# Performance work log

Hardware: AMD Instinct MI355X
Metric: run time of the kernel (lower is better)

## Reference

```python
import jax, jax.numpy as jnp
import numpy as np

HEADS = 8
DIM_HEAD = 64


def setup_inputs() -> dict:
    key = jax.random.key(0)
    ks = jax.random.split(key, 8)
    B, L, m = 4, 1024, 64
    Dq, Dc = 512, 256
    inner = HEADS * DIM_HEAD  # 512
    x = jax.random.normal(ks[0], (B, L, Dq), dtype=jnp.float32)
    context = jax.random.normal(ks[1], (B, L, m, Dc), dtype=jnp.float32)
    mask = jax.random.randint(ks[2], (B, L, m), 0, 2).astype(bool)
    # guarantee at least one valid token per (b,l) row
    mask = mask.at[:, :, 0].set(True)
    bias = jax.random.normal(ks[3], (B, L, m), dtype=jnp.float32)
    s = 0.02
    Wq = jax.random.normal(ks[4], (Dq, inner), dtype=jnp.float32) * s
    Wk = jax.random.normal(ks[5], (Dc, inner), dtype=jnp.float32) * s
    Wv = jax.random.normal(ks[6], (Dc, inner), dtype=jnp.float32) * s
    Wo = jax.random.normal(ks[7], (inner, Dq), dtype=jnp.float32) * s
    bo = jnp.zeros((Dq,), dtype=jnp.float32)
    return {"x": x, "context": context, "mask": mask, "bias": bias,
            "Wq": Wq, "Wk": Wk, "Wv": Wv, "Wo": Wo, "bo": bo}


def reference(x, context, mask, bias, Wq, Wk, Wv, Wo, bo):
    B, L, Dq = x.shape
    m = context.shape[2]
    scale = DIM_HEAD ** (-0.5)
    # projections
    Q = (x @ Wq).reshape(B, L, HEADS, DIM_HEAD)                 # b l h d
    K = (context @ Wk).reshape(B, L, m, HEADS, DIM_HEAD)        # b l m h d
    V = (context @ Wv).reshape(B, L, m, HEADS, DIM_HEAD)        # b l m h d
    scores = jnp.einsum('blhd,blmhd->blhm', Q, K) * scale       # b l h m
    scores = scores + bias[:, :, None, :]
    scores = jnp.where(mask[:, :, None, :], scores, -jnp.inf)
    attn = jax.nn.softmax(scores, axis=-1)
    out = jnp.einsum('blhm,blmhd->blhd', attn, V).reshape(B, L, HEADS * DIM_HEAD)
    return out @ Wo + bo
```

## Files before the change

### kernel.cpp

```cpp
#include <hip/hip_runtime.h>
#include <cstddef>


typedef __attribute__((ext_vector_type(8))) short short8;
typedef __attribute__((ext_vector_type(4))) float float4v;

__device__ __forceinline__ short f2bf(float f) {
  unsigned u = __float_as_uint(f);
  return (short)((u + 0x7fffu + ((u >> 16) & 1u)) >> 16);
}

__global__ __launch_bounds__(256) void k_prep(const float* __restrict__ x,
                                              const float* __restrict__ Wq,
                                              const float* __restrict__ Wk,
                                              const float* __restrict__ Wv,
                                              const float* __restrict__ Wo,
                                              short* __restrict__ xb,
                                              short* __restrict__ Wqb,
                                              short* __restrict__ Wkb,
                                              short* __restrict__ Wvb,
                                              short* __restrict__ WoTb) {
  __shared__ short lt[64][72];
  int b = blockIdx.x, t = threadIdx.x;
  if (b < 2560) {
    size_t i4 = ((size_t)b * 256 + t) * 4;
    const float* src; short* dst; size_t off;
    if (i4 < 2097152)      { src = x;  dst = xb;  off = i4; }
    else if (i4 < 2359296) { src = Wq; dst = Wqb; off = i4 - 2097152; }
    else if (i4 < 2490368) { src = Wk; dst = Wkb; off = i4 - 2359296; }
    else                   { src = Wv; dst = Wvb; off = i4 - 2490368; }
    float4 v = *(const float4*)(src + off);
    short4 o; o.x = f2bf(v.x); o.y = f2bf(v.y); o.z = f2bf(v.z); o.w = f2bf(v.w);
    *(short4*)(dst + off) = o;
    return;
  }
  int tile = b - 2560;
  int k0 = (tile >> 3) * 64, n0 = (tile & 7) * 64;
  int rr = t >> 4, cc = t & 15;
#pragma unroll
  for (int p = 0; p < 4; ++p) {
    int k = p * 16 + rr;
    float4 v = *(const float4*)(Wo + (size_t)(k0 + k) * 512 + n0 + cc * 4);
    short4 o; o.x = f2bf(v.x); o.y = f2bf(v.y); o.z = f2bf(v.z); o.w = f2bf(v.w);
    *(short4*)&lt[k][cc * 4] = o;
  }
  __syncthreads();
#pragma unroll
  for (int p = 0; p < 4; ++p) {
    int n = p * 16 + rr;
    short4 o;
    o.x = lt[cc * 4 + 0][n]; o.y = lt[cc * 4 + 1][n];
    o.z = lt[cc * 4 + 2][n]; o.w = lt[cc * 4 + 3][n];
    *(short4*)&WoTb[(size_t)(n0 + n) * 512 + k0 + cc * 4] = o;
  }
}

template<int BN>
__device__ __forceinline__ void mm_body(const short* __restrict__ A,
                                        const short* __restrict__ Bt,
                                        const float* __restrict__ bias,
                                        void* __restrict__ C,
                                        int lda, int ldb, int ldc, int K,
                                        int bShift, int bMask, int bHS, int crossAK,
                                        float scale, int storeMode,
                                        int bn, int bm,
                                        short* __restrict__ As, short* __restrict__ Bs) {
  int t = threadIdx.x;
  int n0 = bn * BN, m0 = bm * 128;
  int hb = n0 >> bShift;
  const short* aBase = A + (size_t)m0 * lda + (size_t)hb * crossAK;
  const short* bBase = Bt + (size_t)(n0 & bMask) * ldb + (size_t)hb * bHS;
  int w = t >> 6, l = t & 63;
  int wm = w & 1, wn = w >> 1;
  int li = l & 15, kq = l >> 4;
  constexpr int NI = BN / 32;
  float4v acc[4][NI];
#pragma unroll
  for (int i = 0; i < 4; ++i)
#pragma unroll
    for (int j = 0; j < NI; ++j) acc[i][j] = (float4v){0.f, 0.f, 0.f, 0.f};

  for (int k0 = 0; k0 < K; k0 += 64) {
    __syncthreads();
#pragma unroll
    for (int p = 0; p < 4; ++p) {
      int i = p * 256 + t, row = i >> 3, kq8 = i & 7;
      *(uint4*)&As[row * 72 + kq8 * 8] = *(const uint4*)(aBase + (size_t)row * lda + k0 + kq8 * 8);
    }
#pragma unroll
    for (int p = 0; p < BN / 32; ++p) {
      int i = p * 256 + t, row = i >> 3, kq8 = i & 7;
      *(uint4*)&Bs[row * 72 + kq8 * 8] = *(const uint4*)(bBase + (size_t)row * ldb + k0 + kq8 * 8);
    }
    __syncthreads();
#pragma unroll
    for (int kk = 0; kk < 2; ++kk) {
      short8 af[4], bfr[NI];
#pragma unroll
      for (int i = 0; i < 4; ++i)
        af[i]  = *(const short8*)&As[(wm * 64 + i * 16 + li) * 72 + kk * 32 + kq * 8];
#pragma unroll
      for (int i = 0; i < NI; ++i)
        bfr[i] = *(const short8*)&Bs[(wn * (BN / 2) + i * 16 + li) * 72 + kk * 32 + kq * 8];
#pragma unroll
      for (int mi = 0; mi < 4; ++mi)
#pragma unroll
        for (int ni = 0; ni < NI; ++ni)
          acc[mi][ni] = __builtin_amdgcn_mfma_f32_16x16x32_bf16(af[mi], bfr[ni], acc[mi][ni], 0, 0, 0);
    }
  }
#pragma unroll
  for (int ni = 0; ni < NI; ++ni) {
    int col = n0 + wn * (BN / 2) + ni * 16 + li;
    float bv = bias ? bias[col] : 0.f;
    if (storeMode == 2) {
      int row0 = m0 + wm * 64 + kq * 4;
#pragma unroll
      for (int mi = 0; mi < 4; ++mi) {
        short4 o;
        o.x = f2bf(fmaf(acc[mi][ni][0], scale, bv));
        o.y = f2bf(fmaf(acc[mi][ni][1], scale, bv));
        o.z = f2bf(fmaf(acc[mi][ni][2], scale, bv));
        o.w = f2bf(fmaf(acc[mi][ni][3], scale, bv));
        *(short4*)&((short*)C)[(size_t)col * ldc + row0 + mi * 16] = o;
      }
    } else {
#pragma unroll
      for (int mi = 0; mi < 4; ++mi)
#pragma unroll
        for (int r = 0; r < 4; ++r) {
          int row = m0 + wm * 64 + mi * 16 + kq * 4 + r;
          float v = fmaf(acc[mi][ni][r], scale, bv);
          if (storeMode) ((short*)C)[(size_t)row * ldc + col] = f2bf(v);
          else           ((float*)C)[(size_t)row * ldc + col] = v;
        }
    }
  }
}

template<int BN>
__global__ __launch_bounds__(256) void k_mm(const short* __restrict__ A,
                                            const short* __restrict__ Bt,
                                            const float* __restrict__ bias,
                                            void* __restrict__ C,
                                            int lda, int ldb, int ldc, int K,
                                            int bShift, int bMask, int bHS, int crossAK,
                                            float scale, int storeMode) {
  __shared__ short As[128 * 72];
  __shared__ short Bs[BN * 72];
  int gx = gridDim.x, gy = gridDim.y;
  int bn = blockIdx.x, bm = blockIdx.y;
  if ((gy & 7) == 0) {
    int f = blockIdx.y * gx + blockIdx.x;
    int xcd = f & 7, j = f >> 3;
    bn = j % gx;
    bm = (j / gx) * 8 + xcd;
  }
  mm_body<BN>(A, Bt, bias, C, lda, ldb, ldc, K, bShift, bMask, bHS, crossAK,
              scale, storeMode, bn, bm, As, Bs);
}

__global__ __launch_bounds__(256) void k_mm_dual(const short* __restrict__ A0,
                                                 const short* __restrict__ Bt0,
                                                 void* __restrict__ C0, int ldc0,
                                                 float sc0, int md0,
                                                 const short* __restrict__ A1,
                                                 const short* __restrict__ Bt1,
                                                 void* __restrict__ C1, int ldc1,
                                                 float sc1, int md1) {
  __shared__ short As[128 * 72];
  __shared__ short Bs[64 * 72];
  int f = blockIdx.y * 32 + blockIdx.x;
  int xcd = f & 7, bn = f >> 3;
  if (xcd < 4)
    mm_body<64>(A0, Bt0, nullptr, C0, 512, 512, ldc0, 64, 8, 255, 64, 64,
                sc0, md0, bn, xcd, As, Bs);
  else
    mm_body<64>(A1, Bt1, nullptr, C1, 512, 512, ldc1, 64, 8, 255, 64, 64,
                sc1, md1, bn, xcd - 4, As, Bs);
}

__global__ __launch_bounds__(256, 4) void k_attn(const float* __restrict__ ctx,
                                                 const short* __restrict__ Qkb,
                                                 const float* __restrict__ bias,
                                                 const int* __restrict__ mask,
                                                 short* __restrict__ CA) {
  __shared__ __align__(16) short uni[256 * 72];
  __shared__ __align__(16) float S[64][9];
  __shared__ __align__(16) short attn_b[8][72];
  __shared__ float bs[64];
  __shared__ int   msk[64];

  int t = threadIdx.x;
  int r = blockIdx.x;
  int l = t & 63, w = t >> 6;
  int li = l & 15, kq = l >> 4;

  const float* ctxr = ctx + (size_t)r * 16384;
  const short* qrow = Qkb + (size_t)r * 2048;

  int hq = l & 7;
  short8 qf[8];
#pragma unroll
  for (int ks = 0; ks < 8; ++ks)
    qf[ks] = *(const short8*)(qrow + hq * 256 + ks * 32 + kq * 8);

  if (t < 64) { bs[t] = bias[(size_t)r * 64 + t]; msk[t] = mask[(size_t)r * 64 + t]; }

  short (*mc)[264] = (short (*)[264])uni;
  short (*cm)[72]  = (short (*)[72])uni;

  short4 sv[16];
#pragma unroll
  for (int i = 0; i < 16; ++i) {
    int m = w * 16 + i;
    float4 v = *(const float4*)(ctxr + m * 256 + l * 4);
    short4 b4; b4.x = f2bf(v.x); b4.y = f2bf(v.y); b4.z = f2bf(v.z); b4.w = f2bf(v.w);
    sv[i] = b4;
    *(short4*)&mc[m][l * 4] = b4;
  }
  __syncthreads();

  float4v sacc = (float4v){0.f, 0.f, 0.f, 0.f};
#pragma unroll
  for (int ks = 0; ks < 8; ++ks) {
    short8 af = *(const short8*)&mc[w * 16 + li][ks * 32 + kq * 8];
    sacc = __builtin_amdgcn_mfma_f32_16x16x32_bf16(af, qf[ks], sacc, 0, 0, 0);
  }
  if (li < 8) {
#pragma unroll
    for (int rg = 0; rg < 4; ++rg) S[w * 16 + kq * 4 + rg][li] = sacc[rg];
  }
  __syncthreads();

  int m_ = t & 63, h0 = t >> 6;
  bool valid = msk[m_] != 0;
  float b = bs[m_];
  float s0 = valid ? S[m_][h0] + b : -INFINITY;
  float s1 = valid ? S[m_][h0 + 4] + b : -INFINITY;
  float mx0 = s0, mx1 = s1;
#pragma unroll
  for (int o = 32; o > 0; o >>= 1) {
    mx0 = fmaxf(mx0, __shfl_xor(mx0, o, 64));
    mx1 = fmaxf(mx1, __shfl_xor(mx1, o, 64));
  }
  float e0 = __expf(s0 - mx0), e1 = __expf(s1 - mx1);
  float sm0 = e0, sm1 = e1;
#pragma unroll
  for (int o = 32; o > 0; o >>= 1) {
    sm0 += __shfl_xor(sm0, o, 64);
    sm1 += __shfl_xor(sm1, o, 64);
  }
  attn_b[h0][m_]     = f2bf(e0 / sm0);
  attn_b[h0 + 4][m_] = f2bf(e1 / sm1);

#pragma unroll
  for (int p = 0; p < 4; ++p) {
    int c  = l + p * 64;
    int sl = (l >> 2) + p * 16;
#pragma unroll
    for (int k = 0; k < 4; ++k) {
      int wd[4];
#pragma unroll
      for (int j = 0; j < 4; ++j) {
        int2 two = *(int2*)&sv[4 * k + j];
        int wx = __shfl(two.x, sl, 64);
        int wy = __shfl(two.y, sl, 64);
        wd[j] = (l & 2) ? wy : wx;
      }
      short4 o;
      o.x = (l & 1) ? (short)(wd[0] >> 16) : (short)wd[0];
      o.y = (l & 1) ? (short)(wd[1] >> 16) : (short)wd[1];
      o.z = (l & 1) ? (short)(wd[2] >> 16) : (short)wd[2];
      o.w = (l & 1) ? (short)(wd[3] >> 16) : (short)wd[3];
      *(short4*)&cm[c][w * 16 + k * 4] = o;
    }
  }
  __syncthreads();

  short8 bfr[2];
#pragma unroll
  for (int ks = 0; ks < 2; ++ks)
    bfr[ks] = *(const short8*)&attn_b[li & 7][ks * 32 + kq * 8];
  float4v ca[4];
#pragma unroll
  for (int mi = 0; mi < 4; ++mi) ca[mi] = (float4v){0.f, 0.f, 0.f, 0.f};
#pragma unroll
  for (int mi = 0; mi < 4; ++mi)
#pragma unroll
    for (int ks = 0; ks < 2; ++ks) {
      short8 af = *(const short8*)&cm[w * 64 + mi * 16 + li][ks * 32 + kq * 8];
      ca[mi] = __builtin_amdgcn_mfma_f32_16x16x32_bf16(af, bfr[ks], ca[mi], 0, 0, 0);
    }
  short* car = CA + (size_t)r * 2048;
  if (li < 8) {
#pragma unroll
    for (int mi = 0; mi < 4; ++mi)
#pragma unroll
      for (int rg = 0; rg < 4; ++rg)
        car[li * 256 + w * 64 + mi * 16 + kq * 4 + rg] = f2bf(ca[mi][rg]);
  }
}

extern "C" void kernel_launch(void* const* d_in, const int* in_sizes, int n_in,
                              void* d_out, int out_size, void* d_ws, size_t ws_size,
                              hipStream_t stream) {
  const float* x    = (const float*)d_in[0];
  const float* ctx  = (const float*)d_in[1];
  const int*   mask = (const int*)d_in[2];
  const float* bias = (const float*)d_in[3];
  const float* Wq   = (const float*)d_in[4];
  const float* Wk   = (const float*)d_in[5];
  const float* Wv   = (const float*)d_in[6];
  const float* Wo   = (const float*)d_in[7];
  const float* bo   = (const float*)d_in[8];
  float* out = (float*)d_out;

  char* ws = (char*)d_ws;
  short* xb    = (short*)(ws);
  short* Qkb   = (short*)(ws + (4u << 20));
  short* CAb   = (short*)(ws + (20u << 20));
  short* WoTb  = (short*)(ws + (36u << 20));
  short* Wqb   = (short*)(ws + (36u << 20) + (512u << 10));
  short* Wkb   = (short*)(ws + (37u << 20));
  short* Wvb   = (short*)(ws + (37u << 20) + (256u << 10));
  short* WvoTb = (short*)(ws + (38u << 20));
  short* WqkTb = (short*)(ws + (40u << 20));

  k_prep<<<dim3(2624), dim3(256), 0, stream>>>(x, Wq, Wk, Wv, Wo, xb, Wqb, Wkb, Wvb, WoTb);
  k_mm_dual<<<dim3(32, 8), dim3(256), 0, stream>>>(WoTb, Wvb, WvoTb, 2048, 1.0f, 1,
                                                   Wqb, Wkb, WqkTb, 512, 0.125f, 2);
  k_mm<128><<<dim3(16, 32), dim3(256), 0, stream>>>(xb, WqkTb, (const float*)nullptr, Qkb,
                                                    512, 512, 2048, 512, 31, 0x7fffffff, 0, 0, 1.0f, 1);
  k_attn<<<dim3(4096), dim3(256), 0, stream>>>(ctx, Qkb, bias, mask, CAb);
  k_mm<64><<<dim3(8, 32), dim3(256), 0, stream>>>(CAb, WvoTb, bo, out,
                                                  2048, 2048, 512, 2048, 31, 0x7fffffff, 0, 0, 1.0f, 0);
}
```

Measured before the change: 444.4 us.

## Fuse weight-product GEMMs into prep kernel and use direct global-to-LDS loads

The separate kernel that formed the combined Wo·Wv and Wq·Wk bf16 weight products is removed. The prep kernel now reads the fp32 weights directly, converts them while filling LDS, and computes the products itself. This drops one launch and the intermediate bf16 weight buffers. The main GEMM kernel now stages tiles with global_load_lds 16-byte DMA instead of going through registers. That change forces an unpadded 64-element LDS row stride, which may bring back LDS bank conflicts on the fragment reads.

```diff
diff --git a/kernel.cpp b/kernel.cpp
--- a/kernel.cpp
+++ b/kernel.cpp
@@ -8,6 +8,99 @@
 __device__ __forceinline__ short f2bf(float f) {
   unsigned u = __float_as_uint(f);
   return (short)((u + 0x7fffu + ((u >> 16) & 1u)) >> 16);
+}
+
+#define GLDS16(g, l) __builtin_amdgcn_global_load_lds(                         \
+    (const __attribute__((address_space(1))) unsigned int*)(g),                \
+    (__attribute__((address_space(3))) unsigned int*)(l), 16, 0, 0)
+
+__device__ __forceinline__ void mm_body_f32(const float* __restrict__ Af,
+                                            const float* __restrict__ Bf,
+                                            void* __restrict__ C,
+                                            int ldc, int aTrans, int hb,
+                                            float scale, int storeMode,
+                                            int bn, int bm,
+                                            short* __restrict__ As,
+                                            short* __restrict__ Bs) {
+  int t = threadIdx.x;
+  int n0 = bn * 64, m0 = bm * 128;
+  int w = t >> 6, l = t & 63;
+  int wm = w & 1, wn = w >> 1;
+  int li = l & 15, kq = l >> 4;
+#pragma unroll
+  for (int p = 0; p < 4; ++p) {
+    int i = p * 256 + t, row = i >> 3, kq8 = i & 7;
+    float v[8];
+    if (aTrans) {
+#pragma unroll
+      for (int j = 0; j < 8; ++j)
+        v[j] = Af[(size_t)(hb * 64 + kq8 * 8 + j) * 512 + m0 + row];
+    } else {
+      float4 a0 = *(const float4*)(Af + (size_t)(m0 + row) * 512 + hb * 64 + kq8 * 8);
+      float4 a1 = *(const float4*)(Af + (size_t)(m0 + row) * 512 + hb * 64 + kq8 * 8 + 4);
+      v[0] = a0.x; v[1] = a0.y; v[2] = a0.z; v[3] = a0.w;
+      v[4] = a1.x; v[5] = a1.y; v[6] = a1.z; v[7] = a1.w;
+    }
+    short s8[8];
+#pragma unroll
+    for (int j = 0; j < 8; ++j) s8[j] = f2bf(v[j]);
+    *(uint4*)&As[row * 72 + kq8 * 8] = *(uint4*)s8;
+  }
+#pragma unroll
+  for (int p = 0; p < 2; ++p) {
+    int i = p * 256 + t, row = i >> 3, kq8 = i & 7;
+    float4 b0 = *(const float4*)(Bf + (size_t)(n0 % 256 + row) * 512 + hb * 64 + kq8 * 8);
+    float4 b1 = *(const float4*)(Bf + (size_t)(n0 % 256 + row) * 512 + hb * 64 + kq8 * 8 + 4);
+    short s8[8];
+    s8[0] = f2bf(b0.x); s8[1] = f2bf(b0.y); s8[2] = f2bf(b0.z); s8[3] = f2bf(b0.w);
+    s8[4] = f2bf(b1.x); s8[5] = f2bf(b1.y); s8[6] = f2bf(b1.z); s8[7] = f2bf(b1.w);
+    *(uint4*)&Bs[row * 72 + kq8 * 8] = *(uint4*)s8;
+  }
+  __syncthreads();
+  float4v acc[4][2];
+#pragma unroll
+  for (int i = 0; i < 4; ++i)
+#pragma unroll
+    for (int j = 0; j < 2; ++j) acc[i][j] = (float4v){0.f, 0.f, 0.f, 0.f};
+#pragma unroll
+  for (int kk = 0; kk < 2; ++kk) {
+    short8 af[4], bfr[2];
+#pragma unroll
+    for (int i = 0; i < 4; ++i)
+      af[i]  = *(const short8*)&As[(wm * 64 + i * 16 + li) * 72 + kk * 32 + kq * 8];
+#pragma unroll
+    for (int i = 0; i < 2; ++i)
+      bfr[i] = *(const short8*)&Bs[(wn * 32 + i * 16 + li) * 72 + kk * 32 + kq * 8];
+#pragma unroll
+    for (int mi = 0; mi < 4; ++mi)
+#pragma unroll
+      for (int ni = 0; ni < 2; ++ni)
+        acc[mi][ni] = __builtin_amdgcn_mfma_f32_16x16x32_bf16(af[mi], bfr[ni], acc[mi][ni], 0, 0, 0);
+  }
+#pragma unroll
+  for (int ni = 0; ni < 2; ++ni) {
+    int col = n0 + wn * 32 + ni * 16 + li;
+    if (storeMode == 2) {
+      int row0 = m0 + wm * 64 + kq * 4;
+#pragma unroll
+      for (int mi = 0; mi < 4; ++mi) {
+        short4 o;
+        o.x = f2bf(acc[mi][ni][0] * scale);
+        o.y = f2bf(acc[mi][ni][1] * scale);
+        o.z = f2bf(acc[mi][ni][2] * scale);
+        o.w = f2bf(acc[mi][ni][3] * scale);
+        *(short4*)&((short*)C)[(size_t)col * ldc + row0 + mi * 16] = o;
+      }
+    } else {
+#pragma unroll
+      for (int mi = 0; mi < 4; ++mi)
+#pragma unroll
+        for (int r = 0; r < 4; ++r) {
+          int row = m0 + wm * 64 + mi * 16 + kq * 4 + r;
+          ((short*)C)[(size_t)row * ldc + col] = f2bf(acc[mi][ni][r] * scale);
+        }
+    }
+  }
 }
 
 __global__ __launch_bounds__(256) void k_prep(const float* __restrict__ x,
@@ -16,60 +109,41 @@
                                               const float* __restrict__ Wv,
                                               const float* __restrict__ Wo,
                                               short* __restrict__ xb,
-                                              short* __restrict__ Wqb,
-                                              short* __restrict__ Wkb,
-                                              short* __restrict__ Wvb,
-                                              short* __restrict__ WoTb) {
-  __shared__ short lt[64][72];
+                                              short* __restrict__ WvoTb,
+                                              short* __restrict__ WqkTb) {
+  __shared__ __align__(16) short As[128 * 72];
+  __shared__ __align__(16) short Bs[64 * 72];
   int b = blockIdx.x, t = threadIdx.x;
-  if (b < 2560) {
+  if (b < 2048) {
     size_t i4 = ((size_t)b * 256 + t) * 4;
-    const float* src; short* dst; size_t off;
-    if (i4 < 2097152)      { src = x;  dst = xb;  off = i4; }
-    else if (i4 < 2359296) { src = Wq; dst = Wqb; off = i4 - 2097152; }
-    else if (i4 < 2490368) { src = Wk; dst = Wkb; off = i4 - 2359296; }
-    else                   { src = Wv; dst = Wvb; off = i4 - 2490368; }
-    float4 v = *(const float4*)(src + off);
+    float4 v = *(const float4*)(x + i4);
     short4 o; o.x = f2bf(v.x); o.y = f2bf(v.y); o.z = f2bf(v.z); o.w = f2bf(v.w);
-    *(short4*)(dst + off) = o;
+    *(short4*)(xb + i4) = o;
     return;
   }
-  int tile = b - 2560;
-  int k0 = (tile >> 3) * 64, n0 = (tile & 7) * 64;
-  int rr = t >> 4, cc = t & 15;
-#pragma unroll
-  for (int p = 0; p < 4; ++p) {
-    int k = p * 16 + rr;
-    float4 v = *(const float4*)(Wo + (size_t)(k0 + k) * 512 + n0 + cc * 4);
-    short4 o; o.x = f2bf(v.x); o.y = f2bf(v.y); o.z = f2bf(v.z); o.w = f2bf(v.w);
-    *(short4*)&lt[k][cc * 4] = o;
-  }
-  __syncthreads();
-#pragma unroll
-  for (int p = 0; p < 4; ++p) {
-    int n = p * 16 + rr;
-    short4 o;
-    o.x = lt[cc * 4 + 0][n]; o.y = lt[cc * 4 + 1][n];
-    o.z = lt[cc * 4 + 2][n]; o.w = lt[cc * 4 + 3][n];
-    *(short4*)&WoTb[(size_t)(n0 + n) * 512 + k0 + cc * 4] = o;
-  }
+  int f = b - 2048;
+  int xcd = f & 7, bn = f >> 3;
+  int hb = (bn * 64) >> 8;
+  if (xcd < 4)
+    mm_body_f32(Wo, Wv, WvoTb, 2048, 1, hb, 1.0f, 1, bn, xcd, As, Bs);
+  else
+    mm_body_f32(Wq, Wk, WqkTb, 512, 0, hb, 0.125f, 2, bn, xcd - 4, As, Bs);
 }
 
 template<int BN>
-__device__ __forceinline__ void mm_body(const short* __restrict__ A,
-                                        const short* __restrict__ Bt,
-                                        const float* __restrict__ bias,
-                                        void* __restrict__ C,
-                                        int lda, int ldb, int ldc, int K,
-                                        int bShift, int bMask, int bHS, int crossAK,
-                                        float scale, int storeMode,
-                                        int bn, int bm,
-                                        short* __restrict__ As, short* __restrict__ Bs) {
+__device__ __forceinline__ void mm_body_dma(const short* __restrict__ A,
+                                            const short* __restrict__ Bt,
+                                            const float* __restrict__ bias,
+                                            void* __restrict__ C,
+                                            int lda, int ldb, int ldc, int K,
+                                            float scale, int storeBF16,
+                                            int bn, int bm,
+                                            short* __restrict__ As,
+                                            short* __restrict__ Bs) {
   int t = threadIdx.x;
   int n0 = bn * BN, m0 = bm * 128;
-  int hb = n0 >> bShift;
-  const short* aBase = A + (size_t)m0 * lda + (size_t)hb * crossAK;
-  const short* bBase = Bt + (size_t)(n0 & bMask) * ldb + (size_t)hb * bHS;
+  const short* aBase = A + (size_t)m0 * lda;
+  const short* bBase = Bt + (size_t)n0 * ldb;
   int w = t >> 6, l = t & 63;
   int wm = w & 1, wn = w >> 1;
   int li = l & 15, kq = l >> 4;
@@ -84,13 +158,13 @@
     __syncthreads();
 #pragma unroll
     for (int p = 0; p < 4; ++p) {
-      int i = p * 256 + t, row = i >> 3, kq8 = i & 7;
-      *(uint4*)&As[row * 72 + kq8 * 8] = *(const uint4*)(aBase + (size_t)row * lda + k0 + kq8 * 8);
+      int i = p * 256 + t, row = i >> 3, sl = i & 7;
+      GLDS16(aBase + (size_t)row * lda + k0 + sl * 8, &As[i * 8]);
     }
 #pragma unroll
     for (int p = 0; p < BN / 32; ++p) {
-      int i = p * 256 + t, row = i >> 3, kq8 = i & 7;
-      *(uint4*)&Bs[row * 72 + kq8 * 8] = *(const uint4*)(bBase + (size_t)row * ldb + k0 + kq8 * 8);
+      int i = p * 256 + t, row = i >> 3, sl = i & 7;
+      GLDS16(bBase + (size_t)row * ldb + k0 + sl * 8, &Bs[i * 8]);
     }
     __syncthreads();
 #pragma unroll
@@ -98,10 +172,10 @@
       short8 af[4], bfr[NI];
 #pragma unroll
       for (int i = 0; i < 4; ++i)
-        af[i]  = *(const short8*)&As[(wm * 64 + i * 16 + li) * 72 + kk * 32 + kq * 8];
+        af[i]  = *(const short8*)&As[(wm * 64 + i * 16 + li) * 64 + kk * 32 + kq * 8];
 #pragma unroll
       for (int i = 0; i < NI; ++i)
-        bfr[i] = *(const short8*)&Bs[(wn * (BN / 2) + i * 16 + li) * 72 + kk * 32 + kq * 8];
+        bfr[i] = *(const short8*)&Bs[(wn * (BN / 2) + i * 16 + li) * 64 + kk * 32 + kq * 8];
 #pragma unroll
       for (int mi = 0; mi < 4; ++mi)
 #pragma unroll
@@ -113,28 +187,15 @@
   for (int ni = 0; ni < NI; ++ni) {
     int col = n0 + wn * (BN / 2) + ni * 16 + li;
     float bv = bias ? bias[col] : 0.f;
-    if (storeMode == 2) {
-      int row0 = m0 + wm * 64 + kq * 4;
-#pragma unroll
-      for (int mi = 0; mi < 4; ++mi) {
-        short4 o;
-        o.x = f2bf(fmaf(acc[mi][ni][0], scale, bv));
-        o.y = f2bf(fmaf(acc[mi][ni][1], scale, bv));
-        o.z = f2bf(fmaf(acc[mi][ni][2], scale, bv));
-        o.w = f2bf(fmaf(acc[mi][ni][3], scale, bv));
-        *(short4*)&((short*)C)[(size_t)col * ldc + row0 + mi * 16] = o;
+#pragma unroll
+    for (int mi = 0; mi < 4; ++mi)
+#pragma unroll
+      for (int r = 0; r < 4; ++r) {
+        int row = m0 + wm * 64 + mi * 16 + kq * 4 + r;
+        float v = fmaf(acc[mi][ni][r], scale, bv);
+        if (storeBF16) ((short*)C)[(size_t)row * ldc + col] = f2bf(v);
+        else           ((float*)C)[(size_t)row * ldc + col] = v;
       }
-    } else {
-#pragma unroll
-      for (int mi = 0; mi < 4; ++mi)
-#pragma unroll
-        for (int r = 0; r < 4; ++r) {
-          int row = m0 + wm * 64 + mi * 16 + kq * 4 + r;
-          float v = fmaf(acc[mi][ni][r], scale, bv);
-          if (storeMode) ((short*)C)[(size_t)row * ldc + col] = f2bf(v);
-          else           ((float*)C)[(size_t)row * ldc + col] = v;
-        }
-    }
   }
 }
 
@@ -144,10 +205,9 @@
                                             const float* __restrict__ bias,
                                             void* __restrict__ C,
                                             int lda, int ldb, int ldc, int K,
-                                            int bShift, int bMask, int bHS, int crossAK,
-                                            float scale, int storeMode) {
-  __shared__ short As[128 * 72];
-  __shared__ short Bs[BN * 72];
+                                            float scale, int storeBF16) {
+  __shared__ __align__(16) short As[128 * 64];
+  __shared__ __align__(16) short Bs[BN * 64];
   int gx = gridDim.x, gy = gridDim.y;
   int bn = blockIdx.x, bm = blockIdx.y;
   if ((gy & 7) == 0) {
@@ -156,28 +216,7 @@
     bn = j % gx;
     bm = (j / gx) * 8 + xcd;
   }
-  mm_body<BN>(A, Bt, bias, C, lda, ldb, ldc, K, bShift, bMask, bHS, crossAK,
-              scale, storeMode, bn, bm, As, Bs);
-}
-
-__global__ __launch_bounds__(256) void k_mm_dual(const short* __restrict__ A0,
-                                                 const short* __restrict__ Bt0,
-                                                 void* __restrict__ C0, int ldc0,
-                                                 float sc0, int md0,
-                                                 const short* __restrict__ A1,
-                                                 const short* __restrict__ Bt1,
-                                                 void* __restrict__ C1, int ldc1,
-                                                 float sc1, int md1) {
-  __shared__ short As[128 * 72];
-  __shared__ short Bs[64 * 72];
-  int f = blockIdx.y * 32 + blockIdx.x;
-  int xcd = f & 7, bn = f >> 3;
-  if (xcd < 4)
-    mm_body<64>(A0, Bt0, nullptr, C0, 512, 512, ldc0, 64, 8, 255, 64, 64,
-                sc0, md0, bn, xcd, As, Bs);
-  else
-    mm_body<64>(A1, Bt1, nullptr, C1, 512, 512, ldc1, 64, 8, 255, 64, 64,
-                sc1, md1, bn, xcd - 4, As, Bs);
+  mm_body_dma<BN>(A, Bt, bias, C, lda, ldb, ldc, K, scale, storeBF16, bn, bm, As, Bs);
 }
 
 __global__ __launch_bounds__(256, 4) void k_attn(const float* __restrict__ ctx,
@@ -320,19 +359,13 @@
   short* xb    = (short*)(ws);
   short* Qkb   = (short*)(ws + (4u << 20));
   short* CAb   = (short*)(ws + (20u << 20));
-  short* WoTb  = (short*)(ws + (36u << 20));
-  short* Wqb   = (short*)(ws + (36u << 20) + (512u << 10));
-  short* Wkb   = (short*)(ws + (37u << 20));
-  short* Wvb   = (short*)(ws + (37u << 20) + (256u << 10));
-  short* WvoTb = (short*)(ws + (38u << 20));
-  short* WqkTb = (short*)(ws + (40u << 20));
-
-  k_prep<<<dim3(2624), dim3(256), 0, stream>>>(x, Wq, Wk, Wv, Wo, xb, Wqb, Wkb, Wvb, WoTb);
-  k_mm_dual<<<dim3(32, 8), dim3(256), 0, stream>>>(WoTb, Wvb, WvoTb, 2048, 1.0f, 1,
-                                                   Wqb, Wkb, WqkTb, 512, 0.125f, 2);
+  short* WvoTb = (short*)(ws + (36u << 20));
+  short* WqkTb = (short*)(ws + (38u << 20));
+
+  k_prep<<<dim3(2304), dim3(256), 0, stream>>>(x, Wq, Wk, Wv, Wo, xb, WvoTb, WqkTb);
   k_mm<128><<<dim3(16, 32), dim3(256), 0, stream>>>(xb, WqkTb, (const float*)nullptr, Qkb,
-                                                    512, 512, 2048, 512, 31, 0x7fffffff, 0, 0, 1.0f, 1);
+                                                    512, 512, 2048, 512, 1.0f, 1);
   k_attn<<<dim3(4096), dim3(256), 0, stream>>>(ctx, Qkb, bias, mask, CAb);
   k_mm<64><<<dim3(8, 32), dim3(256), 0, stream>>>(CAb, WvoTb, bo, out,
-                                                  2048, 2048, 512, 2048, 31, 0x7fffffff, 0, 0, 1.0f, 0);
-}
+                                                  2048, 2048, 512, 2048, 1.0f, 0);
+}
```

After: 450.6 us. About the same (+1.4%).
